# Performance work log

Measured on AMD Instinct MI355X. Metric: run time of the kernel, lower is better.

Reference implementation:

```python
import jax, jax.numpy as jnp
import numpy as np

B = 4096        # number of sets
MAX_N = 64      # max set size (matches max(n) in data)
DIM = 256       # per-element feature dim
W = 32          # weight_dim = sqrt(hidden_dim=1024)


def sinusoid_pe(length, dim):
    # standard transformer sinusoid PE: pe[p,2i]=sin(p/10000^(2i/dim)), pe[p,2i+1]=cos(...)
    pos = jnp.arange(length, dtype=jnp.float32)[:, None]
    i = jnp.arange(dim)[None, :]
    angle = pos / jnp.power(10000.0, (2.0 * (i // 2)).astype(jnp.float32) / dim)
    return jnp.where(i % 2 == 0, jnp.sin(angle), jnp.cos(angle))


def setup_inputs() -> dict:
    key = jax.random.key(0)
    ks = jax.random.split(key, 6)
    # ragged batch: alternating set sizes 32 and 64, 2048 each -> 196608 rows
    counts = np.tile(np.array([32, 64], dtype=np.int64), B // 2)
    batch = jnp.asarray(np.repeat(np.arange(B, dtype=np.int64), counts))
    N = int(counts.sum())
    x = jax.random.normal(ks[0], (N, DIM), dtype=jnp.float32)
    s = 1.0 / np.sqrt(DIM)
    Wk = jax.random.normal(ks[1], (W, DIM), dtype=jnp.float32) * s
    Wv = jax.random.normal(ks[2], (W, DIM), dtype=jnp.float32) * s
    Wq = jax.random.normal(ks[3], (W, DIM), dtype=jnp.float32) * s
    Wmap = jax.random.normal(ks[4], (DIM, W), dtype=jnp.float32) / np.sqrt(W)
    bmap = jax.random.normal(ks[5], (DIM,), dtype=jnp.float32) * 0.01
    return {"x": x, "batch": batch, "Wk": Wk, "Wv": Wv, "Wq": Wq, "Wmap": Wmap, "bmap": bmap}


def reference(x, batch, Wk, Wv, Wq, Wmap, bmap):
    N = x.shape[0]
    # set sizes and within-set positions (vectorized replacement of torch python loops)
    n = jax.ops.segment_sum(jnp.ones((N,), jnp.int32), batch, num_segments=B)
    ptr = jnp.concatenate([jnp.zeros((1,), jnp.int32), jnp.cumsum(n)])[:-1]
    pos_in_set = jnp.arange(N, dtype=jnp.int32) - ptr[batch]

    # --- Encoder ---
    xmat = jnp.zeros((B, MAX_N, DIM), x.dtype).at[batch, pos_in_set].set(x)
    mask = jnp.zeros((B, MAX_N), bool).at[batch, pos_in_set].set(True)
    pe = sinusoid_pe(MAX_N, DIM)                       # [MAX_N, DIM]
    xpos = xmat + pe[None]                             # [B, MAX_N, DIM]
    m = mask[..., None].astype(x.dtype)
    yk = jnp.einsum('bnd,wd->bnw', xpos, Wk) * m       # [B, MAX_N, W]
    yv = jnp.einsum('bnd,wd->bnw', xpos, Wv) * m
    # z_mat[b,i,j] = sum_n yv[b,n,i] * yk[b,n,j]
    z_mat = jnp.einsum('bnj,bni->bij', yk, yv)         # [B, W, W]

    # --- Decoder ---
    query = sinusoid_pe(MAX_N, DIM) @ Wq.T             # [MAX_N, W]
    decoded = jnp.einsum('mk,bkv->bmv', query, z_mat)  # [B, MAX_N, W]
    x_padded = decoded @ Wmap.T + bmap                 # [B, MAX_N, DIM]
    # unpad: gather valid rows back to flat ragged layout
    x_out = x_padded[batch, pos_in_set]                # [N, DIM]
    return (x_out, batch)
```

## Files before the change

kernel.cpp:

```cpp
#include <hip/hip_runtime.h>
#include <math.h>

#define N_SETS 4096
#define SETS_PER_BLOCK 8
#define GRID_MAIN (N_SETS / SETS_PER_BLOCK)

typedef _Float16 f16;
typedef __attribute__((ext_vector_type(8))) _Float16 f16x8;
typedef __attribute__((ext_vector_type(4))) _Float16 f16x4;
typedef __attribute__((ext_vector_type(4))) float     f32x4;

#define WS_PE    0
#define WS_QH    65536
#define WS_WKV   69632
#define WS_WMAPH 102400
#define WS_PEH   118784
#define WS_PTR   151552

__global__ void k_aux1(const int* __restrict__ batch, float* __restrict__ out2,
                       int* __restrict__ ptr, int N, float* __restrict__ pe) {
    int blk = blockIdx.x;
    if (blk < 768) {
        int i = blk * 256 + threadIdx.x;
        if (i >= N) return;
        int b = batch[i];
        out2[i] = (float)b;
        if (i == 0 || batch[i - 1] != b) ptr[b] = i;
        if (i == N - 1) ptr[N_SETS] = N;
    } else {
        int idx = (blk - 768) * 256 + threadIdx.x;
        int p = idx >> 8, i = idx & 255;
        float e   = (float)(2 * (i / 2)) / 256.0f;
        float inv = powf(10000.0f, -e);
        float ang = (float)p * inv;
        pe[idx] = (i & 1) ? cosf(ang) : sinf(ang);
    }
}

__global__ void k_aux2(const float* __restrict__ Wk, const float* __restrict__ Wv,
                       const float* __restrict__ Wq, const float* __restrict__ Wmap,
                       const float* __restrict__ pe, f16* __restrict__ wkv,
                       f16* __restrict__ wmaph, f16* __restrict__ peh,
                       f16* __restrict__ qh) {
    int blk = blockIdx.x;
    if (blk < 96) {
        int idx = blk * 256 + threadIdx.x;
        if (idx < 16384) {
            int j = idx >> 8, d = idx & 255;
            float v = (j < 32) ? Wk[j * 256 + d] : Wv[(j - 32) * 256 + d];
            wkv[idx] = (f16)v;
        } else {
            int i2 = idx - 16384;
            wmaph[i2] = (f16)Wmap[i2];
        }
    } else if (blk < 160) {
        int idx = (blk - 96) * 256 + threadIdx.x;
        peh[idx] = (f16)pe[idx];
    } else {
        int idx = (blk - 160) * 256 + threadIdx.x;
        int pos = idx >> 5, k = idx & 31;
        const float* pr = pe + pos * 256;
        const float* wr = Wq + k * 256;
        float s = 0.f;
        for (int d = 0; d < 256; d += 4) {
            float4 a = *(const float4*)(pr + d);
            float4 b = *(const float4*)(wr + d);
            s += a.x * b.x + a.y * b.y + a.z * b.z + a.w * b.w;
        }
        qh[idx] = (f16)s;
    }
}

__global__ __launch_bounds__(256, 2) void k_main(
        const float* __restrict__ x,     const f16* __restrict__ wkv,
        const f16* __restrict__ wmaph,   const f16* __restrict__ qh,
        const f16* __restrict__ peh,     const float* __restrict__ bmap,
        const int* __restrict__ ptr,     float* __restrict__ out) {
    __shared__ char lds[59392];

    const int t    = threadIdx.x;
    const int wv   = t >> 6;
    const int l15  = t & 15;
    const int lhi  = (t & 63) >> 4;
    const int arow = 16 * wv + l15;

    int pv[SETS_PER_BLOCK + 1];
    #pragma unroll
    for (int i = 0; i <= SETS_PER_BLOCK; ++i)
        pv[i] = ptr[blockIdx.x * SETS_PER_BLOCK + i];

    #pragma unroll
    for (int i2 = 0; i2 < 8; ++i2) {
        int c = t + 256 * i2;
        int j = c >> 5, d0 = (c & 31) * 8;
        f16x8 w8 = *(const f16x8*)(wkv + j * 256 + d0);
        *(f16x8*)(lds + ((j * 512 + d0 * 2) ^ ((j & 7) << 4))) = w8;
    }
    #pragma unroll
    for (int i2 = 0; i2 < 4; ++i2) {
        int c = t + 256 * i2;
        int d = c >> 2, v0 = (c & 3) * 8;
        f16x8 w8 = *(const f16x8*)(wmaph + d * 32 + v0);
        *(f16x8*)(lds + 32768 + ((d * 64 + v0 * 2) ^ ((d & 7) << 4))) = w8;
    }
    f16x8 pef[8];
    #pragma unroll
    for (int ks = 0; ks < 8; ++ks)
        pef[ks] = *(const f16x8*)(peh + arow * 256 + ks * 32 + lhi * 8);
    const f16x8 qreg = *(const f16x8*)(qh + arow * 32 + lhi * 8);
    float bm[16];
    #pragma unroll
    for (int nt = 0; nt < 16; ++nt) bm[nt] = bmap[16 * nt + l15];

    float4 xf[16];
    {
        const int s0 = pv[0], n0 = pv[1] - pv[0];
        if (arow < n0) {
            const float* xr = x + (size_t)(s0 + arow) * 256 + lhi * 8;
            #pragma unroll
            for (int ks = 0; ks < 8; ++ks) {
                xf[2 * ks]     = *(const float4*)(xr + ks * 32);
                xf[2 * ks + 1] = *(const float4*)(xr + ks * 32 + 4);
            }
        }
    }
    __syncthreads();

    for (int si = 0; si < SETS_PER_BLOCK; ++si) {
        const int s = pv[si], n = pv[si + 1] - s;
        const int n32 = (n + 31) & ~31;

        f16x8 areg[8];
        if (arow < n) {
            #pragma unroll
            for (int ks = 0; ks < 8; ++ks) {
                float4 a = xf[2 * ks], a2 = xf[2 * ks + 1];
                f16x8 h;
                h[0]=(f16)a.x;  h[1]=(f16)a.y;  h[2]=(f16)a.z;  h[3]=(f16)a.w;
                h[4]=(f16)a2.x; h[5]=(f16)a2.y; h[6]=(f16)a2.z; h[7]=(f16)a2.w;
                areg[ks] = h + pef[ks];
            }
        } else {
            #pragma unroll
            for (int ks = 0; ks < 8; ++ks) {
                f16x8 h;
                #pragma unroll
                for (int ii = 0; ii < 8; ++ii) h[ii] = (f16)0.f;
                areg[ks] = h;
            }
        }
        if (si + 1 < SETS_PER_BLOCK) {
            const int s1 = pv[si + 1], n1 = pv[si + 2] - pv[si + 1];
            if (arow < n1) {
                const float* xr = x + (size_t)(s1 + arow) * 256 + lhi * 8;
                #pragma unroll
                for (int ks = 0; ks < 8; ++ks) {
                    xf[2 * ks]     = *(const float4*)(xr + ks * 32);
                    xf[2 * ks + 1] = *(const float4*)(xr + ks * 32 + 4);
                }
            }
        }

        if (16 * wv < n32) {
            f32x4 acc[4];
            #pragma unroll
            for (int nt = 0; nt < 4; ++nt) acc[nt] = (f32x4){0.f, 0.f, 0.f, 0.f};
            #pragma unroll
            for (int ks = 0; ks < 8; ++ks) {
                #pragma unroll
                for (int nt = 0; nt < 4; ++nt) {
                    f16x8 bf = *(const f16x8*)(lds +
                        (((16 * nt + l15) * 512 + ks * 64 + lhi * 16) ^ ((l15 & 7) << 4)));
                    acc[nt] = __builtin_amdgcn_mfma_f32_16x16x32_f16(areg[ks], bf, acc[nt], 0, 0, 0);
                }
            }
            const int row0 = 16 * wv + lhi * 4;
            #pragma unroll
            for (int nt = 0; nt < 4; ++nt) {
                const int col = 16 * nt + l15;
                f16x4 h4;
                #pragma unroll
                for (int q = 0; q < 4; ++q) h4[q] = (f16)acc[nt][q];
                *(f16x4*)(lds + 49152 + ((col * 128 + row0 * 2) ^ ((col & 7) << 4))) = h4;
            }
        }
        __syncthreads();

        {
            const int it = wv >> 1, jt = wv & 1;
            f32x4 zacc = {0.f, 0.f, 0.f, 0.f};
            const int nks = n32 >> 5;
            for (int ks = 0; ks < nks; ++ks) {
                const int r2 = ks * 64 + lhi * 16;
                f16x8 av = *(const f16x8*)(lds + 49152 +
                    (((32 + 16 * it + l15) * 128 + r2) ^ ((l15 & 7) << 4)));
                f16x8 bk = *(const f16x8*)(lds + 49152 +
                    (((16 * jt + l15) * 128 + r2) ^ ((l15 & 7) << 4)));
                zacc = __builtin_amdgcn_mfma_f32_16x16x32_f16(av, bk, zacc, 0, 0, 0);
            }
            const int zc = 16 * jt + l15, zr0 = 16 * it + lhi * 4;
            f16x4 h4;
            #pragma unroll
            for (int q = 0; q < 4; ++q) h4[q] = (f16)zacc[q];
            *(f16x4*)(lds + 57344 + ((zc * 64 + zr0 * 2) ^ ((zc & 3) << 4))) = h4;
        }
        __syncthreads();

        if (16 * wv < n) {
            const int k2 = lhi * 16;
            f16x8 bz0 = *(const f16x8*)(lds + 57344 + ((l15 * 64 + k2) ^ ((l15 & 3) << 4)));
            f16x8 bz1 = *(const f16x8*)(lds + 57344 + (((16 + l15) * 64 + k2) ^ ((l15 & 3) << 4)));
            f32x4 dd0 = {0.f, 0.f, 0.f, 0.f}, dd1 = {0.f, 0.f, 0.f, 0.f};
            dd0 = __builtin_amdgcn_mfma_f32_16x16x32_f16(qreg, bz0, dd0, 0, 0, 0);
            dd1 = __builtin_amdgcn_mfma_f32_16x16x32_f16(qreg, bz1, dd1, 0, 0, 0);
            #pragma unroll
            for (int q = 0; q < 4; ++q) {
                const int m = 16 * wv + lhi * 4 + q;
                *(f16*)(lds + 49152 + ((m * 64 + l15 * 2) ^ ((m & 7) << 4)))            = (f16)dd0[q];
                *(f16*)(lds + 49152 + ((m * 64 + (16 + l15) * 2) ^ ((m & 7) << 4)))     = (f16)dd1[q];
            }
        }
        __syncthreads();

        if (16 * wv < n) {
            const int k2 = lhi * 16;
            f16x8 ad = *(const f16x8*)(lds + 49152 +
                (((16 * wv + l15) * 64 + k2) ^ ((l15 & 7) << 4)));
            const int row0 = 16 * wv + lhi * 4;
            float* orow = out + (size_t)s * 256;
            #pragma unroll
            for (int nt = 0; nt < 16; ++nt) {
                const int dcol = 16 * nt + l15;
                f16x8 bw = *(const f16x8*)(lds + 32768 + ((dcol * 64 + k2) ^ ((l15 & 7) << 4)));
                f32x4 o = {0.f, 0.f, 0.f, 0.f};
                o = __builtin_amdgcn_mfma_f32_16x16x32_f16(ad, bw, o, 0, 0, 0);
                #pragma unroll
                for (int q = 0; q < 4; ++q) {
                    const int row = row0 + q;
                    if (row < n) orow[(size_t)row * 256 + dcol] = o[q] + bm[nt];
                }
            }
        }
        __syncthreads();
    }
}

extern "C" void kernel_launch(void* const* d_in, const int* in_sizes, int n_in,
                              void* d_out, int out_size, void* d_ws, size_t ws_size,
                              hipStream_t stream) {
    const float* x    = (const float*)d_in[0];
    const int*   batch= (const int*)  d_in[1];
    const float* Wk   = (const float*)d_in[2];
    const float* Wv   = (const float*)d_in[3];
    const float* Wq   = (const float*)d_in[4];
    const float* Wmap = (const float*)d_in[5];
    const float* bmap = (const float*)d_in[6];
    float* out = (float*)d_out;

    const int N = in_sizes[1];
    float* pe    = (float*)((char*)d_ws + WS_PE);
    f16*   qh    = (f16*)  ((char*)d_ws + WS_QH);
    f16*   wkv   = (f16*)  ((char*)d_ws + WS_WKV);
    f16*   wmaph = (f16*)  ((char*)d_ws + WS_WMAPH);
    f16*   peh   = (f16*)  ((char*)d_ws + WS_PEH);
    int*   ptr   = (int*)  ((char*)d_ws + WS_PTR);
    float* out2  = out + (size_t)N * 256;

    k_aux1<<<832, 256, 0, stream>>>(batch, out2, ptr, N, pe);
    k_aux2<<<168, 256, 0, stream>>>(Wk, Wv, Wq, Wmap, pe, wkv, wmaph, peh, qh);
    k_main<<<GRID_MAIN, 256, 0, stream>>>(x, wkv, wmaph, qh, peh, bmap, ptr, out);
}
```

Measured before the change: 115.2 us.

## Process each set within a single wave, removing block-wide barriers per set

Restructures the main kernel so that each of 8 waves in a 512-thread block handles two whole sets on its own, using a private LDS scratch region. This removes the four __syncthreads per set that the old cooperative 4-wave scheme needed. PE is moved into LDS instead of registers, and the tile count is specialised at compile time for 32- versus 64-row sets. In exchange it drops the prefetch of the next set's x rows, uses 144KB of LDS per block (which may limit occupancy), and serialises more MFMA work per wave.

```diff
diff --git a/kernel.cpp b/kernel.cpp
--- a/kernel.cpp
+++ b/kernel.cpp
@@ -2,13 +2,17 @@
 #include <math.h>
 
 #define N_SETS 4096
-#define SETS_PER_BLOCK 8
+#define WAVES 8
+#define SPW 2
+#define SETS_PER_BLOCK (WAVES * SPW)
 #define GRID_MAIN (N_SETS / SETS_PER_BLOCK)
 
 typedef _Float16 f16;
 typedef __attribute__((ext_vector_type(8))) _Float16 f16x8;
 typedef __attribute__((ext_vector_type(4))) _Float16 f16x4;
 typedef __attribute__((ext_vector_type(4))) float     f32x4;
+
+template <int V> struct IC { static constexpr int value = V; };
 
 #define WS_PE    0
 #define WS_QH    65536
@@ -71,177 +75,175 @@
     }
 }
 
-__global__ __launch_bounds__(256, 2) void k_main(
+__global__ __launch_bounds__(512, 2) void k_main(
         const float* __restrict__ x,     const f16* __restrict__ wkv,
         const f16* __restrict__ wmaph,   const f16* __restrict__ qh,
         const f16* __restrict__ peh,     const float* __restrict__ bmap,
         const int* __restrict__ ptr,     float* __restrict__ out) {
-    __shared__ char lds[59392];
-
-    const int t    = threadIdx.x;
-    const int wv   = t >> 6;
-    const int l15  = t & 15;
-    const int lhi  = (t & 63) >> 4;
-    const int arow = 16 * wv + l15;
-
-    int pv[SETS_PER_BLOCK + 1];
-    #pragma unroll
-    for (int i = 0; i <= SETS_PER_BLOCK; ++i)
-        pv[i] = ptr[blockIdx.x * SETS_PER_BLOCK + i];
-
-    #pragma unroll
-    for (int i2 = 0; i2 < 8; ++i2) {
-        int c = t + 256 * i2;
+    __shared__ char lds[147456];
+
+    const int t   = threadIdx.x;
+    const int wid = t >> 6;
+    const int l15 = t & 15;
+    const int lhi = (t & 63) >> 4;
+    char* wlds = lds + 81920 + (wid << 13);
+
+    #pragma unroll
+    for (int i = 0; i < 4; ++i) {
+        int c = t + 512 * i;
         int j = c >> 5, d0 = (c & 31) * 8;
-        f16x8 w8 = *(const f16x8*)(wkv + j * 256 + d0);
-        *(f16x8*)(lds + ((j * 512 + d0 * 2) ^ ((j & 7) << 4))) = w8;
-    }
-    #pragma unroll
-    for (int i2 = 0; i2 < 4; ++i2) {
-        int c = t + 256 * i2;
+        *(f16x8*)(lds + ((j * 512 + d0 * 2) ^ ((j & 7) << 4))) =
+            *(const f16x8*)(wkv + j * 256 + d0);
+    }
+    #pragma unroll
+    for (int i = 0; i < 2; ++i) {
+        int c = t + 512 * i;
         int d = c >> 2, v0 = (c & 3) * 8;
-        f16x8 w8 = *(const f16x8*)(wmaph + d * 32 + v0);
-        *(f16x8*)(lds + 32768 + ((d * 64 + v0 * 2) ^ ((d & 7) << 4))) = w8;
-    }
-    f16x8 pef[8];
-    #pragma unroll
-    for (int ks = 0; ks < 8; ++ks)
-        pef[ks] = *(const f16x8*)(peh + arow * 256 + ks * 32 + lhi * 8);
-    const f16x8 qreg = *(const f16x8*)(qh + arow * 32 + lhi * 8);
+        *(f16x8*)(lds + 32768 + ((d * 64 + v0 * 2) ^ ((d & 7) << 4))) =
+            *(const f16x8*)(wmaph + d * 32 + v0);
+    }
+    #pragma unroll
+    for (int i = 0; i < 4; ++i) {
+        int c = t + 512 * i;
+        int j = c >> 5, d0 = (c & 31) * 8;
+        *(f16x8*)(lds + 49152 + ((j * 512 + d0 * 2) ^ ((j & 7) << 4))) =
+            *(const f16x8*)(peh + j * 256 + d0);
+    }
+    f16x8 qregs[4];
+    #pragma unroll
+    for (int mt = 0; mt < 4; ++mt)
+        qregs[mt] = *(const f16x8*)(qh + (16 * mt + l15) * 32 + lhi * 8);
     float bm[16];
     #pragma unroll
     for (int nt = 0; nt < 16; ++nt) bm[nt] = bmap[16 * nt + l15];
-
-    float4 xf[16];
-    {
-        const int s0 = pv[0], n0 = pv[1] - pv[0];
-        if (arow < n0) {
-            const float* xr = x + (size_t)(s0 + arow) * 256 + lhi * 8;
-            #pragma unroll
-            for (int ks = 0; ks < 8; ++ks) {
-                xf[2 * ks]     = *(const float4*)(xr + ks * 32);
-                xf[2 * ks + 1] = *(const float4*)(xr + ks * 32 + 4);
-            }
-        }
-    }
     __syncthreads();
 
-    for (int si = 0; si < SETS_PER_BLOCK; ++si) {
-        const int s = pv[si], n = pv[si + 1] - s;
-        const int n32 = (n + 31) & ~31;
-
-        f16x8 areg[8];
-        if (arow < n) {
-            #pragma unroll
-            for (int ks = 0; ks < 8; ++ks) {
-                float4 a = xf[2 * ks], a2 = xf[2 * ks + 1];
-                f16x8 h;
-                h[0]=(f16)a.x;  h[1]=(f16)a.y;  h[2]=(f16)a.z;  h[3]=(f16)a.w;
-                h[4]=(f16)a2.x; h[5]=(f16)a2.y; h[6]=(f16)a2.z; h[7]=(f16)a2.w;
-                areg[ks] = h + pef[ks];
-            }
-        } else {
+    const int g0 = blockIdx.x * SETS_PER_BLOCK + wid * SPW;
+    int s, n;
+
+    auto process = [&](auto nmtc) {
+        constexpr int NMT = decltype(nmtc)::value;
+        const int swz7 = (l15 & 7) << 4;
+
+        #pragma unroll
+        for (int mt = 0; mt < NMT; ++mt) {
+            const int arow = 16 * mt + l15;
+            const bool act = arow < n;
+            float4 raw[16];
+            const float* xr = x + (size_t)(s + arow) * 256 + lhi * 8;
+            if (act) {
+                #pragma unroll
+                for (int ks = 0; ks < 8; ++ks) {
+                    raw[2 * ks]     = *(const float4*)(xr + ks * 32);
+                    raw[2 * ks + 1] = *(const float4*)(xr + ks * 32 + 4);
+                }
+            }
+            f16x8 areg[8];
             #pragma unroll
             for (int ks = 0; ks < 8; ++ks) {
                 f16x8 h;
-                #pragma unroll
-                for (int ii = 0; ii < 8; ++ii) h[ii] = (f16)0.f;
+                if (act) {
+                    float4 a = raw[2 * ks], a2 = raw[2 * ks + 1];
+                    h[0]=(f16)a.x;  h[1]=(f16)a.y;  h[2]=(f16)a.z;  h[3]=(f16)a.w;
+                    h[4]=(f16)a2.x; h[5]=(f16)a2.y; h[6]=(f16)a2.z; h[7]=(f16)a2.w;
+                    f16x8 pef = *(const f16x8*)(lds + 49152 +
+                        ((arow * 512 + (ks * 32 + lhi * 8) * 2) ^ swz7));
+                    h = h + pef;
+                } else {
+                    #pragma unroll
+                    for (int ii = 0; ii < 8; ++ii) h[ii] = (f16)0.f;
+                }
                 areg[ks] = h;
             }
-        }
-        if (si + 1 < SETS_PER_BLOCK) {
-            const int s1 = pv[si + 1], n1 = pv[si + 2] - pv[si + 1];
-            if (arow < n1) {
-                const float* xr = x + (size_t)(s1 + arow) * 256 + lhi * 8;
+            #pragma unroll
+            for (int nt = 0; nt < 4; ++nt) {
+                f32x4 acc = {0.f, 0.f, 0.f, 0.f};
+                const int brow = 16 * nt + l15;
                 #pragma unroll
                 for (int ks = 0; ks < 8; ++ks) {
-                    xf[2 * ks]     = *(const float4*)(xr + ks * 32);
-                    xf[2 * ks + 1] = *(const float4*)(xr + ks * 32 + 4);
-                }
-            }
-        }
-
-        if (16 * wv < n32) {
-            f32x4 acc[4];
-            #pragma unroll
-            for (int nt = 0; nt < 4; ++nt) acc[nt] = (f32x4){0.f, 0.f, 0.f, 0.f};
-            #pragma unroll
-            for (int ks = 0; ks < 8; ++ks) {
-                #pragma unroll
-                for (int nt = 0; nt < 4; ++nt) {
                     f16x8 bf = *(const f16x8*)(lds +
-                        (((16 * nt + l15) * 512 + ks * 64 + lhi * 16) ^ ((l15 & 7) << 4)));
-                    acc[nt] = __builtin_amdgcn_mfma_f32_16x16x32_f16(areg[ks], bf, acc[nt], 0, 0, 0);
-                }
-            }
-            const int row0 = 16 * wv + lhi * 4;
-            #pragma unroll
-            for (int nt = 0; nt < 4; ++nt) {
+                        ((brow * 512 + ks * 64 + lhi * 16) ^ swz7));
+                    acc = __builtin_amdgcn_mfma_f32_16x16x32_f16(areg[ks], bf, acc, 0, 0, 0);
+                }
                 const int col = 16 * nt + l15;
+                const int row0 = 16 * mt + lhi * 4;
                 f16x4 h4;
                 #pragma unroll
-                for (int q = 0; q < 4; ++q) h4[q] = (f16)acc[nt][q];
-                *(f16x4*)(lds + 49152 + ((col * 128 + row0 * 2) ^ ((col & 7) << 4))) = h4;
-            }
-        }
-        __syncthreads();
-
-        {
-            const int it = wv >> 1, jt = wv & 1;
+                for (int q = 0; q < 4; ++q) h4[q] = (f16)acc[q];
+                *(f16x4*)(wlds + ((col * 128 + row0 * 2) ^ swz7)) = h4;
+            }
+        }
+
+        f32x4 zt[4];
+        #pragma unroll
+        for (int ij = 0; ij < 4; ++ij) {
+            const int it = ij >> 1, jt = ij & 1;
             f32x4 zacc = {0.f, 0.f, 0.f, 0.f};
-            const int nks = n32 >> 5;
-            for (int ks = 0; ks < nks; ++ks) {
+            const int ca = 32 + 16 * it + l15, cb = 16 * jt + l15;
+            #pragma unroll
+            for (int ks = 0; ks < NMT / 2; ++ks) {
                 const int r2 = ks * 64 + lhi * 16;
-                f16x8 av = *(const f16x8*)(lds + 49152 +
-                    (((32 + 16 * it + l15) * 128 + r2) ^ ((l15 & 7) << 4)));
-                f16x8 bk = *(const f16x8*)(lds + 49152 +
-                    (((16 * jt + l15) * 128 + r2) ^ ((l15 & 7) << 4)));
+                f16x8 av = *(const f16x8*)(wlds + ((ca * 128 + r2) ^ swz7));
+                f16x8 bk = *(const f16x8*)(wlds + ((cb * 128 + r2) ^ swz7));
                 zacc = __builtin_amdgcn_mfma_f32_16x16x32_f16(av, bk, zacc, 0, 0, 0);
             }
-            const int zc = 16 * jt + l15, zr0 = 16 * it + lhi * 4;
+            zt[ij] = zacc;
+        }
+        #pragma unroll
+        for (int ij = 0; ij < 4; ++ij) {
+            const int zc = 16 * (ij & 1) + l15, zr0 = 16 * (ij >> 1) + lhi * 4;
             f16x4 h4;
             #pragma unroll
-            for (int q = 0; q < 4; ++q) h4[q] = (f16)zacc[q];
-            *(f16x4*)(lds + 57344 + ((zc * 64 + zr0 * 2) ^ ((zc & 3) << 4))) = h4;
-        }
-        __syncthreads();
-
-        if (16 * wv < n) {
-            const int k2 = lhi * 16;
-            f16x8 bz0 = *(const f16x8*)(lds + 57344 + ((l15 * 64 + k2) ^ ((l15 & 3) << 4)));
-            f16x8 bz1 = *(const f16x8*)(lds + 57344 + (((16 + l15) * 64 + k2) ^ ((l15 & 3) << 4)));
-            f32x4 dd0 = {0.f, 0.f, 0.f, 0.f}, dd1 = {0.f, 0.f, 0.f, 0.f};
-            dd0 = __builtin_amdgcn_mfma_f32_16x16x32_f16(qreg, bz0, dd0, 0, 0, 0);
-            dd1 = __builtin_amdgcn_mfma_f32_16x16x32_f16(qreg, bz1, dd1, 0, 0, 0);
-            #pragma unroll
-            for (int q = 0; q < 4; ++q) {
-                const int m = 16 * wv + lhi * 4 + q;
-                *(f16*)(lds + 49152 + ((m * 64 + l15 * 2) ^ ((m & 7) << 4)))            = (f16)dd0[q];
-                *(f16*)(lds + 49152 + ((m * 64 + (16 + l15) * 2) ^ ((m & 7) << 4)))     = (f16)dd1[q];
-            }
-        }
-        __syncthreads();
-
-        if (16 * wv < n) {
-            const int k2 = lhi * 16;
-            f16x8 ad = *(const f16x8*)(lds + 49152 +
-                (((16 * wv + l15) * 64 + k2) ^ ((l15 & 7) << 4)));
-            const int row0 = 16 * wv + lhi * 4;
-            float* orow = out + (size_t)s * 256;
-            #pragma unroll
-            for (int nt = 0; nt < 16; ++nt) {
-                const int dcol = 16 * nt + l15;
-                f16x8 bw = *(const f16x8*)(lds + 32768 + ((dcol * 64 + k2) ^ ((l15 & 7) << 4)));
+            for (int q = 0; q < 4; ++q) h4[q] = (f16)zt[ij][q];
+            *(f16x4*)(wlds + ((zc * 64 + zr0 * 2) ^ ((zc & 3) << 4))) = h4;
+        }
+
+        #pragma unroll
+        for (int nt2 = 0; nt2 < 2; ++nt2) {
+            const int zrow = 16 * nt2 + l15;
+            f16x8 bz = *(const f16x8*)(wlds + ((zrow * 64 + lhi * 16) ^ ((zrow & 3) << 4)));
+            #pragma unroll
+            for (int mt = 0; mt < NMT; ++mt) {
+                f32x4 dd = {0.f, 0.f, 0.f, 0.f};
+                dd = __builtin_amdgcn_mfma_f32_16x16x32_f16(qregs[mt], bz, dd, 0, 0, 0);
+                #pragma unroll
+                for (int q = 0; q < 4; ++q) {
+                    const int m = 16 * mt + lhi * 4 + q;
+                    *(f16*)(wlds + 2048 + ((m * 64 + zrow * 2) ^ ((m & 7) << 4))) = (f16)dd[q];
+                }
+            }
+        }
+
+        f16x8 ad[NMT];
+        #pragma unroll
+        for (int mt = 0; mt < NMT; ++mt) {
+            const int drow = 16 * mt + l15;
+            ad[mt] = *(const f16x8*)(wlds + 2048 + ((drow * 64 + lhi * 16) ^ swz7));
+        }
+        float* ob = out + (size_t)s * 256;
+        #pragma unroll
+        for (int nt = 0; nt < 16; ++nt) {
+            const int dcol = 16 * nt + l15;
+            f16x8 bw = *(const f16x8*)(lds + 32768 + ((dcol * 64 + lhi * 16) ^ swz7));
+            #pragma unroll
+            for (int mt = 0; mt < NMT; ++mt) {
                 f32x4 o = {0.f, 0.f, 0.f, 0.f};
-                o = __builtin_amdgcn_mfma_f32_16x16x32_f16(ad, bw, o, 0, 0, 0);
+                o = __builtin_amdgcn_mfma_f32_16x16x32_f16(ad[mt], bw, o, 0, 0, 0);
+                const int row0 = 16 * mt + lhi * 4;
                 #pragma unroll
                 for (int q = 0; q < 4; ++q) {
                     const int row = row0 + q;
-                    if (row < n) orow[(size_t)row * 256 + dcol] = o[q] + bm[nt];
-                }
-            }
-        }
-        __syncthreads();
+                    if (row < n) ob[(size_t)row * 256 + dcol] = o[q] + bm[nt];
+                }
+            }
+        }
+    };
+
+    for (int sw = 0; sw < SPW; ++sw) {
+        s = ptr[g0 + sw];
+        n = ptr[g0 + sw + 1] - s;
+        if (n > 32) process(IC<4>{});
+        else        process(IC<2>{});
     }
 }
 
@@ -268,5 +270,5 @@
 
     k_aux1<<<832, 256, 0, stream>>>(batch, out2, ptr, N, pe);
     k_aux2<<<168, 256, 0, stream>>>(Wk, Wv, Wq, Wmap, pe, wkv, wmaph, peh, qh);
-    k_main<<<GRID_MAIN, 256, 0, stream>>>(x, wkv, wmaph, qh, peh, bmap, ptr, out);
-}
+    k_main<<<GRID_MAIN, 512, 0, stream>>>(x, wkv, wmaph, qh, peh, bmap, ptr, out);
+}
```

New measurement: 201.0 us. 74.5% more time.

## Split main block into two wave groups processing sets concurrently

Applied to the files above, without the earlier changes.

Doubles the block to 512 threads and splits it into two independent groups of four waves. Each group handles four of the block's eight sets using its own LDS scratch region, while the Wk/Wv and Wmap tiles are loaded once and shared by both groups. Two block-wide barriers are removed where only same-wave data dependencies exist, aiming to cut barrier stalls and serialisation across sets. The tighter launch bound (512, 4) forces a much lower per-thread register budget, which risks spilling the large register-resident x, PE and bias arrays. The larger LDS footprint may also limit how many blocks fit on a CU.

```diff
diff --git a/kernel.cpp b/kernel.cpp
--- a/kernel.cpp
+++ b/kernel.cpp
@@ -71,18 +71,24 @@
     }
 }
 
-__global__ __launch_bounds__(256, 2) void k_main(
+__global__ __launch_bounds__(512, 4) void k_main(
         const float* __restrict__ x,     const f16* __restrict__ wkv,
         const f16* __restrict__ wmaph,   const f16* __restrict__ qh,
         const f16* __restrict__ peh,     const float* __restrict__ bmap,
         const int* __restrict__ ptr,     float* __restrict__ out) {
-    __shared__ char lds[59392];
+    __shared__ char lds[77824];
 
     const int t    = threadIdx.x;
-    const int wv   = t >> 6;
+    const int wid  = t >> 6;
+    const int grp  = wid >> 2;
+    const int wv   = wid & 3;
     const int l15  = t & 15;
     const int lhi  = (t & 63) >> 4;
     const int arow = 16 * wv + l15;
+    const int swz7 = (l15 & 7) << 4;
+    char* ysh = lds + 49152 + grp * 14336;
+    char* zsh = ysh + 8192;
+    char* dsh = ysh + 10240;
 
     int pv[SETS_PER_BLOCK + 1];
     #pragma unroll
@@ -90,18 +96,18 @@
         pv[i] = ptr[blockIdx.x * SETS_PER_BLOCK + i];
 
     #pragma unroll
-    for (int i2 = 0; i2 < 8; ++i2) {
-        int c = t + 256 * i2;
+    for (int i = 0; i < 4; ++i) {
+        int c = t + 512 * i;
         int j = c >> 5, d0 = (c & 31) * 8;
-        f16x8 w8 = *(const f16x8*)(wkv + j * 256 + d0);
-        *(f16x8*)(lds + ((j * 512 + d0 * 2) ^ ((j & 7) << 4))) = w8;
-    }
-    #pragma unroll
-    for (int i2 = 0; i2 < 4; ++i2) {
-        int c = t + 256 * i2;
+        *(f16x8*)(lds + ((j * 512 + d0 * 2) ^ ((j & 7) << 4))) =
+            *(const f16x8*)(wkv + j * 256 + d0);
+    }
+    #pragma unroll
+    for (int i = 0; i < 2; ++i) {
+        int c = t + 512 * i;
         int d = c >> 2, v0 = (c & 3) * 8;
-        f16x8 w8 = *(const f16x8*)(wmaph + d * 32 + v0);
-        *(f16x8*)(lds + 32768 + ((d * 64 + v0 * 2) ^ ((d & 7) << 4))) = w8;
+        *(f16x8*)(lds + 32768 + ((d * 64 + v0 * 2) ^ ((d & 7) << 4))) =
+            *(const f16x8*)(wmaph + d * 32 + v0);
     }
     f16x8 pef[8];
     #pragma unroll
@@ -112,9 +118,10 @@
     #pragma unroll
     for (int nt = 0; nt < 16; ++nt) bm[nt] = bmap[16 * nt + l15];
 
+    const int base = 4 * grp;
     float4 xf[16];
     {
-        const int s0 = pv[0], n0 = pv[1] - pv[0];
+        const int s0 = pv[base], n0 = pv[base + 1] - pv[base];
         if (arow < n0) {
             const float* xr = x + (size_t)(s0 + arow) * 256 + lhi * 8;
             #pragma unroll
@@ -126,8 +133,8 @@
     }
     __syncthreads();
 
-    for (int si = 0; si < SETS_PER_BLOCK; ++si) {
-        const int s = pv[si], n = pv[si + 1] - s;
+    for (int j = 0; j < 4; ++j) {
+        const int s = pv[base + j], n = pv[base + j + 1] - s;
         const int n32 = (n + 31) & ~31;
 
         f16x8 areg[8];
@@ -149,8 +156,8 @@
                 areg[ks] = h;
             }
         }
-        if (si + 1 < SETS_PER_BLOCK) {
-            const int s1 = pv[si + 1], n1 = pv[si + 2] - pv[si + 1];
+        if (j + 1 < 4) {
+            const int s1 = pv[base + j + 1], n1 = pv[base + j + 2] - pv[base + j + 1];
             if (arow < n1) {
                 const float* xr = x + (size_t)(s1 + arow) * 256 + lhi * 8;
                 #pragma unroll
@@ -170,7 +177,7 @@
                 #pragma unroll
                 for (int nt = 0; nt < 4; ++nt) {
                     f16x8 bf = *(const f16x8*)(lds +
-                        (((16 * nt + l15) * 512 + ks * 64 + lhi * 16) ^ ((l15 & 7) << 4)));
+                        (((16 * nt + l15) * 512 + ks * 64 + lhi * 16) ^ swz7));
                     acc[nt] = __builtin_amdgcn_mfma_f32_16x16x32_f16(areg[ks], bf, acc[nt], 0, 0, 0);
                 }
             }
@@ -181,7 +188,7 @@
                 f16x4 h4;
                 #pragma unroll
                 for (int q = 0; q < 4; ++q) h4[q] = (f16)acc[nt][q];
-                *(f16x4*)(lds + 49152 + ((col * 128 + row0 * 2) ^ ((col & 7) << 4))) = h4;
+                *(f16x4*)(ysh + ((col * 128 + row0 * 2) ^ swz7)) = h4;
             }
         }
         __syncthreads();
@@ -189,59 +196,55 @@
         {
             const int it = wv >> 1, jt = wv & 1;
             f32x4 zacc = {0.f, 0.f, 0.f, 0.f};
+            const int ca = 32 + 16 * it + l15, cb = 16 * jt + l15;
             const int nks = n32 >> 5;
             for (int ks = 0; ks < nks; ++ks) {
                 const int r2 = ks * 64 + lhi * 16;
-                f16x8 av = *(const f16x8*)(lds + 49152 +
-                    (((32 + 16 * it + l15) * 128 + r2) ^ ((l15 & 7) << 4)));
-                f16x8 bk = *(const f16x8*)(lds + 49152 +
-                    (((16 * jt + l15) * 128 + r2) ^ ((l15 & 7) << 4)));
+                f16x8 av = *(const f16x8*)(ysh + ((ca * 128 + r2) ^ swz7));
+                f16x8 bk = *(const f16x8*)(ysh + ((cb * 128 + r2) ^ swz7));
                 zacc = __builtin_amdgcn_mfma_f32_16x16x32_f16(av, bk, zacc, 0, 0, 0);
             }
             const int zc = 16 * jt + l15, zr0 = 16 * it + lhi * 4;
             f16x4 h4;
             #pragma unroll
             for (int q = 0; q < 4; ++q) h4[q] = (f16)zacc[q];
-            *(f16x4*)(lds + 57344 + ((zc * 64 + zr0 * 2) ^ ((zc & 3) << 4))) = h4;
+            *(f16x4*)(zsh + ((zc * 64 + zr0 * 2) ^ ((l15 & 3) << 4))) = h4;
         }
         __syncthreads();
 
         if (16 * wv < n) {
             const int k2 = lhi * 16;
-            f16x8 bz0 = *(const f16x8*)(lds + 57344 + ((l15 * 64 + k2) ^ ((l15 & 3) << 4)));
-            f16x8 bz1 = *(const f16x8*)(lds + 57344 + (((16 + l15) * 64 + k2) ^ ((l15 & 3) << 4)));
+            f16x8 bz0 = *(const f16x8*)(zsh + ((l15 * 64 + k2) ^ ((l15 & 3) << 4)));
+            f16x8 bz1 = *(const f16x8*)(zsh + (((16 + l15) * 64 + k2) ^ ((l15 & 3) << 4)));
             f32x4 dd0 = {0.f, 0.f, 0.f, 0.f}, dd1 = {0.f, 0.f, 0.f, 0.f};
             dd0 = __builtin_amdgcn_mfma_f32_16x16x32_f16(qreg, bz0, dd0, 0, 0, 0);
             dd1 = __builtin_amdgcn_mfma_f32_16x16x32_f16(qreg, bz1, dd1, 0, 0, 0);
             #pragma unroll
             for (int q = 0; q < 4; ++q) {
                 const int m = 16 * wv + lhi * 4 + q;
-                *(f16*)(lds + 49152 + ((m * 64 + l15 * 2) ^ ((m & 7) << 4)))            = (f16)dd0[q];
-                *(f16*)(lds + 49152 + ((m * 64 + (16 + l15) * 2) ^ ((m & 7) << 4)))     = (f16)dd1[q];
-            }
-        }
-        __syncthreads();
+                *(f16*)(dsh + ((m * 64 + l15 * 2) ^ ((m & 7) << 4)))        = (f16)dd0[q];
+                *(f16*)(dsh + ((m * 64 + (16 + l15) * 2) ^ ((m & 7) << 4))) = (f16)dd1[q];
+            }
+        }
 
         if (16 * wv < n) {
             const int k2 = lhi * 16;
-            f16x8 ad = *(const f16x8*)(lds + 49152 +
-                (((16 * wv + l15) * 64 + k2) ^ ((l15 & 7) << 4)));
+            f16x8 ad = *(const f16x8*)(dsh + (((16 * wv + l15) * 64 + k2) ^ swz7));
             const int row0 = 16 * wv + lhi * 4;
-            float* orow = out + (size_t)s * 256;
+            float* ob = out + (size_t)s * 256;
             #pragma unroll
             for (int nt = 0; nt < 16; ++nt) {
                 const int dcol = 16 * nt + l15;
-                f16x8 bw = *(const f16x8*)(lds + 32768 + ((dcol * 64 + k2) ^ ((l15 & 7) << 4)));
+                f16x8 bw = *(const f16x8*)(lds + 32768 + ((dcol * 64 + k2) ^ swz7));
                 f32x4 o = {0.f, 0.f, 0.f, 0.f};
                 o = __builtin_amdgcn_mfma_f32_16x16x32_f16(ad, bw, o, 0, 0, 0);
                 #pragma unroll
                 for (int q = 0; q < 4; ++q) {
                     const int row = row0 + q;
-                    if (row < n) orow[(size_t)row * 256 + dcol] = o[q] + bm[nt];
+                    if (row < n) ob[(size_t)row * 256 + dcol] = o[q] + bm[nt];
                 }
             }
         }
-        __syncthreads();
     }
 }
 
@@ -268,5 +271,5 @@
 
     k_aux1<<<832, 256, 0, stream>>>(batch, out2, ptr, N, pe);
     k_aux2<<<168, 256, 0, stream>>>(Wk, Wv, Wq, Wmap, pe, wkv, wmaph, peh, qh);
-    k_main<<<GRID_MAIN, 256, 0, stream>>>(x, wkv, wmaph, qh, peh, bmap, ptr, out);
-}
+    k_main<<<GRID_MAIN, 512, 0, stream>>>(x, wkv, wmaph, qh, peh, bmap, ptr, out);
+}
```

After: 327.8 us. 185% more time.
